# Performance work log

Hardware: AMD Instinct MI355X
Metric: run time of the kernel (lower is better)

Reference implementation:

```python
import jax, jax.numpy as jnp
import numpy as np


def setup_inputs() -> dict:
    key = jax.random.key(0)
    k1, k2, k3 = jax.random.split(key, 3)
    B, N, C, R = 256, 512, 1000, 64
    x = jax.random.normal(k1, (B, N), dtype=jnp.float32)
    # kaiming_uniform_(a=0) on weight [C, R, N]: bound = sqrt(6 / fan_in), fan_in = N
    bound = float(np.sqrt(6.0 / N))
    weight = jax.random.uniform(k2, (C, R, N), dtype=jnp.float32, minval=-bound, maxval=bound)
    # original inits bias to 0, but use random to exercise the subtraction path
    bias = jax.random.normal(k3, (C, N), dtype=jnp.float32) * 0.1
    return {"x": x, "weight": weight, "bias": bias}


def reference(x, weight, bias):
    # x: [B, N]; weight: [C, R, N]; bias: [C, N]
    # Faithful math: s_r[b, c] = W_c @ (x_b - bias_c);  out[b, c] = ||s_r[b, c]||^2
    # Fused form avoiding the [B, C, N] diff blowup:
    #   W_c (x_b - b_c) = (W x)_bc - (W b)_c
    Wx = jnp.einsum("bn,crn->bcr", x, weight)      # [B, C, R]
    Wb = jnp.einsum("cn,crn->cr", bias, weight)    # [C, R]
    s_r = Wx - Wb[None, :, :]                        # [B, C, R]
    out = jnp.sum(s_r * s_r, axis=-1)                # [B, C] squared L2 norm over r
    return out
```

## Files before the change

### kernel.cpp

```cpp
#include <hip/hip_runtime.h>
#include <hip/hip_bf16.h>

#define BDIM 256
#define NDIM 512
#define CDIM 1000
#define RDIM 64
#define BK 64
#define NT (NDIM / BK)

typedef __attribute__((ext_vector_type(4))) float f32x4;
typedef __attribute__((ext_vector_type(8))) short bf16x8;
typedef __attribute__((ext_vector_type(4))) unsigned int u32x4;

__device__ __forceinline__ uint32_t pk2(float lo, float hi) {
    unsigned short l = __builtin_bit_cast(unsigned short, __float2bfloat16(lo));
    unsigned short h = __builtin_bit_cast(unsigned short, __float2bfloat16(hi));
    return ((uint32_t)h << 16) | (uint32_t)l;
}

__device__ __forceinline__ void gload16(const void* g, void* l) {
    __builtin_amdgcn_global_load_lds(
        (const __attribute__((address_space(1))) void*)g,
        (__attribute__((address_space(3))) void*)l, 16, 0, 0);
}

__global__ __launch_bounds__(256)
void Mahalanobis_xconv_kernel(const float* __restrict__ x, uint4* __restrict__ xws)
{
    const int tid = blockIdx.x * 256 + threadIdx.x;
    const int t   = tid >> 11;
    const int rem = tid & 2047;
    const int row = rem >> 3;
    const int sIn = (rem & 7) << 4;
    const int uIn = sIn ^ ((row & 7) << 4);
    const int col0 = t * BK + (uIn >> 1);
    const float4* src = reinterpret_cast<const float4*>(x + (size_t)row * NDIM + col0);
    const float4 a = src[0], b = src[1];
    uint4 pk = {pk2(a.x, a.y), pk2(a.z, a.w), pk2(b.x, b.y), pk2(b.z, b.w)};
    xws[tid] = pk;
}

__global__ __launch_bounds__(256, 2)
void Mahalanobis_72834055405642_kernel(const char* __restrict__ xws,
                                       const float* __restrict__ w,
                                       const float* __restrict__ bias,
                                       float* __restrict__ out)
{
    __shared__ alignas(16) char  lds_x[BDIM * BK * 2];
    __shared__ alignas(16) char  lds_w[128 * BK * 4];
    __shared__ alignas(16) float bias_lds[2 * NDIM];
    __shared__ float sb_lds[128];

    const int tid  = threadIdx.x;
    const int lane = tid & 63;
    const int wv   = tid >> 6;
    const int l15  = lane & 15;
    const int lhi  = lane >> 4;
    const int c0   = blockIdx.x * 2;

    const char* wbytes = reinterpret_cast<const char*>(w) + (size_t)c0 * (RDIM * NDIM * 4);
    const int   winner = (lane & 15) * 16;

    auto issueX = [&](int t) {
        #pragma unroll
        for (int q = 0; q < 8; ++q)
            gload16(xws + (size_t)t * 32768 + wv * 8192 + q * 1024 + (size_t)lane * 16,
                    lds_x + wv * 8192 + q * 1024);
    };
    auto issueW = [&](int t) {
        #pragma unroll
        for (int q = 0; q < 8; ++q) {
            const int row = wv * 32 + q * 4 + (lane >> 4);
            gload16(wbytes + (size_t)row * 2048 + t * 256 + (winner ^ ((row & 7) << 5)),
                    lds_w + wv * 8192 + q * 1024);
        }
    };

    const int swr   = (l15 & 7) << 4;
    const int jrow2 = tid >> 1;
    const int jh    = tid & 1;
    const int swj   = (jrow2 & 7) << 5;

    f32x4 acc[4][8];
    #pragma unroll
    for (int m = 0; m < 4; ++m)
        #pragma unroll
        for (int n = 0; n < 8; ++n)
            acc[m][n] = (f32x4){0.f, 0.f, 0.f, 0.f};

    float sbp = 0.f;

    {
        const f32x4 bv = *reinterpret_cast<const f32x4*>(bias + (size_t)c0 * NDIM + tid * 4);
        *reinterpret_cast<f32x4*>(bias_lds + tid * 4) = bv;
    }

    for (int t = 0; t < NT; ++t) {
        issueX(t);
        issueW(t);
        __syncthreads();

        bf16x8 af[4][2];
        #pragma unroll
        for (int m = 0; m < 4; ++m) {
            const int row = wv * 64 + m * 16 + l15;
            #pragma unroll
            for (int ks = 0; ks < 2; ++ks)
                af[m][ks] = *reinterpret_cast<const bf16x8*>(
                    lds_x + row * 128 + ((ks * 64 + lhi * 16) ^ swr));
        }

        {
            const char*  wp = lds_w + jrow2 * 256;
            const float* bl = bias_lds + (jrow2 >> 6) * NDIM + t * BK + jh * 32;
            #pragma unroll
            for (int i = 0; i < 8; ++i) {
                const f32x4 wv4 = *reinterpret_cast<const f32x4*>(
                    wp + ((jh * 128 + i * 16) ^ swj));
                const f32x4 bv4 = *reinterpret_cast<const f32x4*>(bl + i * 4);
                sbp += wv4[0]*bv4[0] + wv4[1]*bv4[1] + wv4[2]*bv4[2] + wv4[3]*bv4[3];
            }
        }

        #pragma unroll
        for (int ks = 0; ks < 2; ++ks) {
            #pragma unroll
            for (int n = 0; n < 8; ++n) {
                const int row = n * 16 + l15;
                const char* pp = lds_w + row * 256 +
                                 ((ks * 128 + lhi * 32) ^ ((row & 7) << 5));
                const f32x4 wlo = *reinterpret_cast<const f32x4*>(pp);
                const f32x4 whi = *reinterpret_cast<const f32x4*>(pp + 16);
                u32x4 pk = {pk2(wlo[0], wlo[1]), pk2(wlo[2], wlo[3]),
                            pk2(whi[0], whi[1]), pk2(whi[2], whi[3])};
                const bf16x8 bw = __builtin_bit_cast(bf16x8, pk);
                #pragma unroll
                for (int m = 0; m < 4; ++m)
                    acc[m][n] = __builtin_amdgcn_mfma_f32_16x16x32_bf16(
                        af[m][ks], bw, acc[m][n], 0, 0, 0);
            }
        }

        __syncthreads();
    }

    sbp += __shfl_xor(sbp, 1);
    if (jh == 0) sb_lds[jrow2] = sbp;
    __syncthreads();

    float sb[8];
    #pragma unroll
    for (int n = 0; n < 8; ++n) sb[n] = sb_lds[n * 16 + l15];

    #pragma unroll
    for (int m = 0; m < 4; ++m) {
        #pragma unroll
        for (int rg = 0; rg < 4; ++rg) {
            float p0 = 0.f, p1 = 0.f;
            #pragma unroll
            for (int n = 0; n < 4; ++n) {
                const float d0 = acc[m][n][rg]     - sb[n];
                const float d1 = acc[m][n + 4][rg] - sb[n + 4];
                p0 += d0 * d0;
                p1 += d1 * d1;
            }
            #pragma unroll
            for (int s = 1; s < 16; s <<= 1) {
                p0 += __shfl_xor(p0, s);
                p1 += __shfl_xor(p1, s);
            }
            if (l15 == 0) {
                const int b = wv * 64 + m * 16 + lhi * 4 + rg;
                float2 o2 = {p0, p1};
                *reinterpret_cast<float2*>(out + (size_t)b * CDIM + c0) = o2;
            }
        }
    }
}

__global__ __launch_bounds__(256, 4)
void Mahalanobis_fallback_kernel(const float* __restrict__ x,
                                 const float* __restrict__ w,
                                 const float* __restrict__ bias,
                                 float* __restrict__ out)
{
    __shared__ alignas(16) char lds_x[BDIM * BK * 2];
    __shared__ alignas(16) char lds_w[RDIM * BK * 2];
    __shared__ float sb_lds[RDIM];

    const int tid  = threadIdx.x;
    const int lane = tid & 63;
    const int wv   = tid >> 6;
    const int l15  = lane & 15;
    const int lhi  = lane >> 4;
    const int c0   = blockIdx.x;

    const int jrow = tid >> 2;
    const int jq   = tid & 3;
    const float* wbase = w + (size_t)c0 * (RDIM * NDIM) + (size_t)jrow * NDIM + jq * 16;
    const float* bbase = bias + (size_t)c0 * NDIM + jq * 16;

    f32x4 acc[4][4];
    #pragma unroll
    for (int m = 0; m < 4; ++m)
        #pragma unroll
        for (int n = 0; n < 4; ++n)
            acc[m][n] = (f32x4){0.f, 0.f, 0.f, 0.f};

    float sbp = 0.f;
    const int swr = (l15 & 7) << 4;
    const int sww = (jrow & 7) << 4;
    const int xrow = tid >> 2;
    const int xq   = tid & 3;

    for (int t = 0; t < NT; ++t) {
        const float4* wsrc = reinterpret_cast<const float4*>(wbase + t * BK);
        const float4* bsrc = reinterpret_cast<const float4*>(bbase + t * BK);
        float4 w0 = wsrc[0], w1 = wsrc[1], w2 = wsrc[2], w3 = wsrc[3];
        float4 b0 = bsrc[0], b1 = bsrc[1], b2 = bsrc[2], b3 = bsrc[3];

        #pragma unroll
        for (int p = 0; p < 4; ++p) {
            const int r = p * 64 + xrow;
            const float4* s = reinterpret_cast<const float4*>(
                x + (size_t)r * NDIM + t * BK + xq * 16);
            float4 va = s[0], vb = s[1], vc = s[2], vd = s[3];
            uint4 pa = {pk2(va.x, va.y), pk2(va.z, va.w), pk2(vb.x, vb.y), pk2(vb.z, vb.w)};
            uint4 pb = {pk2(vc.x, vc.y), pk2(vc.z, vc.w), pk2(vd.x, vd.y), pk2(vd.z, vd.w)};
            const int sw = (r & 7) << 4;
            char* rowp = lds_x + r * 128;
            *reinterpret_cast<uint4*>(rowp + ((xq * 32) ^ sw))      = pa;
            *reinterpret_cast<uint4*>(rowp + ((xq * 32 + 16) ^ sw)) = pb;
        }

        sbp += w0.x*b0.x + w0.y*b0.y + w0.z*b0.z + w0.w*b0.w
             + w1.x*b1.x + w1.y*b1.y + w1.z*b1.z + w1.w*b1.w
             + w2.x*b2.x + w2.y*b2.y + w2.z*b2.z + w2.w*b2.w
             + w3.x*b3.x + w3.y*b3.y + w3.z*b3.z + w3.w*b3.w;
        {
            char* rowp = lds_w + jrow * 128;
            uint4 pa = {pk2(w0.x, w0.y), pk2(w0.z, w0.w), pk2(w1.x, w1.y), pk2(w1.z, w1.w)};
            uint4 pb = {pk2(w2.x, w2.y), pk2(w2.z, w2.w), pk2(w3.x, w3.y), pk2(w3.z, w3.w)};
            *reinterpret_cast<uint4*>(rowp + ((jq * 32) ^ sww))      = pa;
            *reinterpret_cast<uint4*>(rowp + ((jq * 32 + 16) ^ sww)) = pb;
        }

        __syncthreads();

        #pragma unroll
        for (int ks = 0; ks < 2; ++ks) {
            bf16x8 af[4];
            bf16x8 bfr[4];
            #pragma unroll
            for (int m = 0; m < 4; ++m) {
                const int row = wv * 64 + m * 16 + l15;
                af[m] = *reinterpret_cast<const bf16x8*>(
                    lds_x + row * 128 + ((ks * 64 + lhi * 16) ^ swr));
            }
            #pragma unroll
            for (int n = 0; n < 4; ++n) {
                const int row = n * 16 + l15;
                bfr[n] = *reinterpret_cast<const bf16x8*>(
                    lds_w + row * 128 + ((ks * 64 + lhi * 16) ^ swr));
            }
            #pragma unroll
            for (int m = 0; m < 4; ++m)
                #pragma unroll
                for (int n = 0; n < 4; ++n)
                    acc[m][n] = __builtin_amdgcn_mfma_f32_16x16x32_bf16(
                        af[m], bfr[n], acc[m][n], 0, 0, 0);
        }

        __syncthreads();
    }

    sbp += __shfl_xor(sbp, 1);
    sbp += __shfl_xor(sbp, 2);
    if (jq == 0) sb_lds[jrow] = sbp;
    __syncthreads();

    float sb[4];
    #pragma unroll
    for (int n = 0; n < 4; ++n) sb[n] = sb_lds[n * 16 + l15];

    #pragma unroll
    for (int m = 0; m < 4; ++m) {
        #pragma unroll
        for (int rg = 0; rg < 4; ++rg) {
            float p = 0.f;
            #pragma unroll
            for (int n = 0; n < 4; ++n) {
                const float d = acc[m][n][rg] - sb[n];
                p += d * d;
            }
            #pragma unroll
            for (int s = 1; s < 16; s <<= 1)
                p += __shfl_xor(p, s);
            if (l15 == 0) {
                const int b = wv * 64 + m * 16 + lhi * 4 + rg;
                out[(size_t)b * CDIM + c0] = p;
            }
        }
    }
}

extern "C" void kernel_launch(void* const* d_in, const int* in_sizes, int n_in,
                              void* d_out, int out_size, void* d_ws, size_t ws_size,
                              hipStream_t stream) {
    const float* x    = (const float*)d_in[0];
    const float* w    = (const float*)d_in[1];
    const float* bias = (const float*)d_in[2];
    float* out = (float*)d_out;

    if (ws_size >= (size_t)(BDIM * NDIM * 2)) {
        hipLaunchKernelGGL(Mahalanobis_xconv_kernel, dim3(64), dim3(256), 0, stream,
                           x, (uint4*)d_ws);
        hipLaunchKernelGGL(Mahalanobis_72834055405642_kernel, dim3(CDIM / 2), dim3(256),
                           0, stream, (const char*)d_ws, w, bias, out);
    } else {
        hipLaunchKernelGGL(Mahalanobis_fallback_kernel, dim3(CDIM), dim3(256),
                           0, stream, x, w, bias, out);
    }
}
```

Measured before the change: 42.35 us.

## Process four classes per 512-thread block to share the x tile across waves

Each block now handles four classes instead of two and runs 512 threads as eight waves. The waves split into two batch halves times four classes, so each wave computes 128 batch rows for one class. The goal is to reuse the staged bf16 x tile across more classes and halve the x loads per class. In exchange the grid shrinks to 250 blocks and LDS per block rises to roughly 105KB, which likely allows only one block per CU and leaves a few CUs idle.

```diff
diff --git a/kernel.cpp b/kernel.cpp
--- a/kernel.cpp
+++ b/kernel.cpp
@@ -7,6 +7,7 @@
 #define RDIM 64
 #define BK 64
 #define NT (NDIM / BK)
+#define NCLS 4
 
 typedef __attribute__((ext_vector_type(4))) float f32x4;
 typedef __attribute__((ext_vector_type(8))) short bf16x8;
@@ -40,32 +41,34 @@
     xws[tid] = pk;
 }
 
-__global__ __launch_bounds__(256, 2)
+__global__ __launch_bounds__(512, 2)
 void Mahalanobis_72834055405642_kernel(const char* __restrict__ xws,
                                        const float* __restrict__ w,
                                        const float* __restrict__ bias,
                                        float* __restrict__ out)
 {
     __shared__ alignas(16) char  lds_x[BDIM * BK * 2];
-    __shared__ alignas(16) char  lds_w[128 * BK * 4];
-    __shared__ alignas(16) float bias_lds[2 * NDIM];
-    __shared__ float sb_lds[128];
+    __shared__ alignas(16) char  lds_w[NCLS * RDIM * BK * 4];
+    __shared__ alignas(16) float bias_lds[NCLS * NDIM];
+    __shared__ float sb_lds[NCLS * RDIM];
 
     const int tid  = threadIdx.x;
     const int lane = tid & 63;
     const int wv   = tid >> 6;
     const int l15  = lane & 15;
     const int lhi  = lane >> 4;
-    const int c0   = blockIdx.x * 2;
+    const int mr   = wv >> 2;
+    const int cl   = wv & 3;
+    const int c0   = blockIdx.x * NCLS;
 
     const char* wbytes = reinterpret_cast<const char*>(w) + (size_t)c0 * (RDIM * NDIM * 4);
     const int   winner = (lane & 15) * 16;
 
     auto issueX = [&](int t) {
         #pragma unroll
-        for (int q = 0; q < 8; ++q)
-            gload16(xws + (size_t)t * 32768 + wv * 8192 + q * 1024 + (size_t)lane * 16,
-                    lds_x + wv * 8192 + q * 1024);
+        for (int q = 0; q < 4; ++q)
+            gload16(xws + (size_t)t * 32768 + wv * 4096 + q * 1024 + (size_t)lane * 16,
+                    lds_x + wv * 4096 + q * 1024);
     };
     auto issueW = [&](int t) {
         #pragma unroll
@@ -76,16 +79,15 @@
         }
     };
 
-    const int swr   = (l15 & 7) << 4;
     const int jrow2 = tid >> 1;
     const int jh    = tid & 1;
     const int swj   = (jrow2 & 7) << 5;
 
-    f32x4 acc[4][8];
-    #pragma unroll
-    for (int m = 0; m < 4; ++m)
-        #pragma unroll
-        for (int n = 0; n < 8; ++n)
+    f32x4 acc[8][4];
+    #pragma unroll
+    for (int m = 0; m < 8; ++m)
+        #pragma unroll
+        for (int n = 0; n < 4; ++n)
             acc[m][n] = (f32x4){0.f, 0.f, 0.f, 0.f};
 
     float sbp = 0.f;
@@ -99,16 +101,6 @@
         issueX(t);
         issueW(t);
         __syncthreads();
-
-        bf16x8 af[4][2];
-        #pragma unroll
-        for (int m = 0; m < 4; ++m) {
-            const int row = wv * 64 + m * 16 + l15;
-            #pragma unroll
-            for (int ks = 0; ks < 2; ++ks)
-                af[m][ks] = *reinterpret_cast<const bf16x8*>(
-                    lds_x + row * 128 + ((ks * 64 + lhi * 16) ^ swr));
-        }
 
         {
             const char*  wp = lds_w + jrow2 * 256;
@@ -124,9 +116,16 @@
 
         #pragma unroll
         for (int ks = 0; ks < 2; ++ks) {
-            #pragma unroll
-            for (int n = 0; n < 8; ++n) {
-                const int row = n * 16 + l15;
+            bf16x8 af[8];
+            #pragma unroll
+            for (int m = 0; m < 8; ++m) {
+                const int row = mr * 128 + m * 16 + l15;
+                af[m] = *reinterpret_cast<const bf16x8*>(
+                    lds_x + row * 128 + ((ks * 64 + lhi * 16) ^ ((row & 7) << 4)));
+            }
+            #pragma unroll
+            for (int n = 0; n < 4; ++n) {
+                const int row = cl * RDIM + n * 16 + l15;
                 const char* pp = lds_w + row * 256 +
                                  ((ks * 128 + lhi * 32) ^ ((row & 7) << 5));
                 const f32x4 wlo = *reinterpret_cast<const f32x4*>(pp);
@@ -135,9 +134,9 @@
                             pk2(whi[0], whi[1]), pk2(whi[2], whi[3])};
                 const bf16x8 bw = __builtin_bit_cast(bf16x8, pk);
                 #pragma unroll
-                for (int m = 0; m < 4; ++m)
+                for (int m = 0; m < 8; ++m)
                     acc[m][n] = __builtin_amdgcn_mfma_f32_16x16x32_bf16(
-                        af[m][ks], bw, acc[m][n], 0, 0, 0);
+                        af[m], bw, acc[m][n], 0, 0, 0);
             }
         }
 
@@ -148,31 +147,26 @@
     if (jh == 0) sb_lds[jrow2] = sbp;
     __syncthreads();
 
-    float sb[8];
-    #pragma unroll
-    for (int n = 0; n < 8; ++n) sb[n] = sb_lds[n * 16 + l15];
-
-    #pragma unroll
-    for (int m = 0; m < 4; ++m) {
+    float sb[4];
+    #pragma unroll
+    for (int n = 0; n < 4; ++n) sb[n] = sb_lds[cl * RDIM + n * 16 + l15];
+
+    #pragma unroll
+    for (int m = 0; m < 8; ++m) {
         #pragma unroll
         for (int rg = 0; rg < 4; ++rg) {
-            float p0 = 0.f, p1 = 0.f;
+            float p = 0.f;
             #pragma unroll
             for (int n = 0; n < 4; ++n) {
-                const float d0 = acc[m][n][rg]     - sb[n];
-                const float d1 = acc[m][n + 4][rg] - sb[n + 4];
-                p0 += d0 * d0;
-                p1 += d1 * d1;
-            }
-            #pragma unroll
-            for (int s = 1; s < 16; s <<= 1) {
-                p0 += __shfl_xor(p0, s);
-                p1 += __shfl_xor(p1, s);
-            }
+                const float d = acc[m][n][rg] - sb[n];
+                p += d * d;
+            }
+            #pragma unroll
+            for (int s = 1; s < 16; s <<= 1)
+                p += __shfl_xor(p, s);
             if (l15 == 0) {
-                const int b = wv * 64 + m * 16 + lhi * 4 + rg;
-                float2 o2 = {p0, p1};
-                *reinterpret_cast<float2*>(out + (size_t)b * CDIM + c0) = o2;
+                const int b = mr * 128 + m * 16 + lhi * 4 + rg;
+                out[(size_t)b * CDIM + c0 + cl] = p;
             }
         }
     }
@@ -315,7 +309,7 @@
     if (ws_size >= (size_t)(BDIM * NDIM * 2)) {
         hipLaunchKernelGGL(Mahalanobis_xconv_kernel, dim3(64), dim3(256), 0, stream,
                            x, (uint4*)d_ws);
-        hipLaunchKernelGGL(Mahalanobis_72834055405642_kernel, dim3(CDIM / 2), dim3(256),
+        hipLaunchKernelGGL(Mahalanobis_72834055405642_kernel, dim3(CDIM / NCLS), dim3(512),
                            0, stream, (const char*)d_ws, w, bias, out);
     } else {
         hipLaunchKernelGGL(Mahalanobis_fallback_kernel, dim3(CDIM), dim3(256),
```

New measurement: 47.85 us. +13.0%, slower.
